# Kernel tuning notes

Hardware: AMD Instinct MI355X
Metric: run time of the kernel (lower is better)

Reference implementation:

```python
import jax, jax.numpy as jnp
import numpy as np


def _log_g(x):
    # log_g(x) = log(relu(x)+1) if x >= 0 else x
    return jnp.where(x >= 0, jnp.log1p(jnp.maximum(x, 0.0)), x)


def _min_gru(hg):
    # hg: [B, H, L] -> [B, H/2, L]
    h, gate = jnp.split(hg, 2, axis=1)
    log_coeffs = -jax.nn.softplus(gate)                    # log(1 - z)
    log_values = -jax.nn.softplus(-gate) + _log_g(h)       # log(z) + log g(h)
    a_star = jnp.cumsum(log_coeffs, axis=2)
    log_h0_plus_b_star = jax.lax.cumlogsumexp(log_values - a_star, axis=2)
    return jnp.exp(a_star + log_h0_plus_b_star)


def setup_inputs() -> dict:
    key = jax.random.key(0)
    B, H, L = 8, 512, 8192
    x = jax.random.normal(key, (B, H, L), dtype=jnp.float32)
    return {"x": x}


def reference(x) -> jnp.ndarray:
    # bidirectional minGRU: forward scan on first half of channels,
    # reversed scan on second half.
    fore, back = jnp.split(x, 2, axis=1)
    out_fore = _min_gru(fore)
    out_back = jnp.flip(_min_gru(jnp.flip(back, axis=2)), axis=2)
    return jnp.concatenate([out_fore, out_back], axis=1)  # [B, H/2, L]
```

## Files before the change

kernel.cpp:

```cpp
#include <hip/hip_runtime.h>
#include <math.h>


#define SEQ_L 8192
#define NTHREADS 256
#define PER_THREAD 8
#define TILE (NTHREADS * PER_THREAD)
#define NTILES (SEQ_L / TILE)

__global__ __launch_bounds__(NTHREADS) void mingru_scan_kernel(
    const float* __restrict__ x, float* __restrict__ out) {
    const int blk = blockIdx.x;
    const int dir = blk >> 10;
    const int s   = blk & 1023;
    const int b   = s >> 7;
    const int c   = s & 127;

    const int tid  = threadIdx.x;
    const int lane = tid & 63;
    const int wave = tid >> 6;

    const float* __restrict__ hrow = x + (size_t)((b * 512) + (dir * 256) + c) * SEQ_L;
    const float* __restrict__ grow = x + (size_t)((b * 512) + (dir * 256) + 128 + c) * SEQ_L;
    float* __restrict__ orow = out + (size_t)((b * 256) + (dir * 128) + c) * SEQ_L;

    __shared__ float sA[4];
    __shared__ float sB[4];

    float carry = 0.0f;

    for (int tile = 0; tile < NTILES; ++tile) {
        const int base = tile * TILE + tid * PER_THREAD;

        float hv[PER_THREAD], gv[PER_THREAD];
        if (dir == 0) {
            float4 h0 = *(const float4*)(hrow + base);
            float4 h1 = *(const float4*)(hrow + base + 4);
            float4 g0 = *(const float4*)(grow + base);
            float4 g1 = *(const float4*)(grow + base + 4);
            hv[0]=h0.x; hv[1]=h0.y; hv[2]=h0.z; hv[3]=h0.w;
            hv[4]=h1.x; hv[5]=h1.y; hv[6]=h1.z; hv[7]=h1.w;
            gv[0]=g0.x; gv[1]=g0.y; gv[2]=g0.z; gv[3]=g0.w;
            gv[4]=g1.x; gv[5]=g1.y; gv[6]=g1.z; gv[7]=g1.w;
        } else {
            const int p = SEQ_L - base - PER_THREAD;
            float4 h0 = *(const float4*)(hrow + p);
            float4 h1 = *(const float4*)(hrow + p + 4);
            float4 g0 = *(const float4*)(grow + p);
            float4 g1 = *(const float4*)(grow + p + 4);
            hv[0]=h1.w; hv[1]=h1.z; hv[2]=h1.y; hv[3]=h1.x;
            hv[4]=h0.w; hv[5]=h0.z; hv[6]=h0.y; hv[7]=h0.x;
            gv[0]=g1.w; gv[1]=g1.z; gv[2]=g1.y; gv[3]=g1.x;
            gv[4]=g0.w; gv[5]=g0.z; gv[6]=g0.y; gv[7]=g0.x;
        }

        float av[PER_THREAD], bv[PER_THREAD];
        float pa = 1.0f, pb = 0.0f;
#pragma unroll
        for (int j = 0; j < PER_THREAD; ++j) {
            const float gt = gv[j];
            const float e  = __expf(-fabsf(gt));
            const float r  = 1.0f / (1.0f + e);
            const float sn = e * r;
            const float sp = r;
            const float z  = (gt >= 0.0f) ? sp : sn;
            const float a  = (gt >= 0.0f) ? sn : sp;
            const float hh = hv[j];
            const float gf = (hh >= 0.0f) ? (hh + 1.0f) : __expf(hh);
            const float bb = z * gf;
            av[j] = a; bv[j] = bb;
            pb = a * pb + bb;
            pa = a * pa;
        }

#pragma unroll
        for (int d = 1; d < 64; d <<= 1) {
            const float oa = __shfl_up(pa, d);
            const float ob = __shfl_up(pb, d);
            if (lane >= d) {
                pb = pa * ob + pb;
                pa = pa * oa;
            }
        }

        if (lane == 63) { sA[wave] = pa; sB[wave] = pb; }
        __syncthreads();

        float st = carry;
        for (int w = 0; w < wave; ++w) st = sA[w] * st + sB[w];
        float ea = __shfl_up(pa, 1);
        float eb = __shfl_up(pb, 1);
        if (lane == 0) { ea = 1.0f; eb = 0.0f; }
        st = ea * st + eb;

        float ov[PER_THREAD];
        float H = st;
#pragma unroll
        for (int j = 0; j < PER_THREAD; ++j) {
            H = av[j] * H + bv[j];
            ov[j] = H;
        }

        if (dir == 0) {
            *(float4*)(orow + base)     = make_float4(ov[0], ov[1], ov[2], ov[3]);
            *(float4*)(orow + base + 4) = make_float4(ov[4], ov[5], ov[6], ov[7]);
        } else {
            const int p = SEQ_L - base - PER_THREAD;
            *(float4*)(orow + p)     = make_float4(ov[7], ov[6], ov[5], ov[4]);
            *(float4*)(orow + p + 4) = make_float4(ov[3], ov[2], ov[1], ov[0]);
        }

        float nc = carry;
#pragma unroll
        for (int w = 0; w < 4; ++w) nc = sA[w] * nc + sB[w];
        carry = nc;
        __syncthreads();
    }
}

extern "C" void kernel_launch(void* const* d_in, const int* in_sizes, int n_in,
                              void* d_out, int out_size, void* d_ws, size_t ws_size,
                              hipStream_t stream) {
    const float* x = (const float*)d_in[0];
    float* out = (float*)d_out;
    mingru_scan_kernel<<<2048, NTHREADS, 0, stream>>>(x, out);
}
```

Measured before the change: 228.5 us.

## Prefetch next tile, double-buffer wave totals, and apply carry with precomputed prefix products

Loads the next tile's h and gate values into registers before computing the current tile, so global memory latency overlaps with the scan math. The per-wave totals in shared memory are double-buffered, which removes the second barrier in each tile iteration. The final pass now uses the stored local prefix values plus carry times the prefix product, replacing a serial recurrence with independent FMAs. In exchange, register pressure rises from holding the prefetched float4s and the extra prefix arrays.

```diff
diff --git a/kernel.cpp b/kernel.cpp
--- a/kernel.cpp
+++ b/kernel.cpp
@@ -21,58 +21,69 @@
     const int wave = tid >> 6;
 
     const float* __restrict__ hrow = x + (size_t)((b * 512) + (dir * 256) + c) * SEQ_L;
-    const float* __restrict__ grow = x + (size_t)((b * 512) + (dir * 256) + 128 + c) * SEQ_L;
+    const float* __restrict__ grow = hrow + (size_t)128 * SEQ_L;
     float* __restrict__ orow = out + (size_t)((b * 256) + (dir * 128) + c) * SEQ_L;
 
-    __shared__ float sA[4];
-    __shared__ float sB[4];
+    __shared__ float sA[2][4];
+    __shared__ float sB[2][4];
 
     float carry = 0.0f;
 
-    for (int tile = 0; tile < NTILES; ++tile) {
-        const int base = tile * TILE + tid * PER_THREAD;
+    {
+    }
+    int base0 = tid * PER_THREAD;
+    int idx0  = dir ? (SEQ_L - base0 - PER_THREAD) : base0;
+    float4 nh0 = *(const float4*)(hrow + idx0);
+    float4 nh1 = *(const float4*)(hrow + idx0 + 4);
+    float4 ng0 = *(const float4*)(grow + idx0);
+    float4 ng1 = *(const float4*)(grow + idx0 + 4);
+
+#pragma unroll
+    for (int t = 0; t < NTILES; ++t) {
+        const float4 h0 = nh0, h1 = nh1, g0 = ng0, g1 = ng1;
+
+        if (t + 1 < NTILES) {
+            const int nb = (t + 1) * TILE + tid * PER_THREAD;
+            const int ni = dir ? (SEQ_L - nb - PER_THREAD) : nb;
+            nh0 = *(const float4*)(hrow + ni);
+            nh1 = *(const float4*)(hrow + ni + 4);
+            ng0 = *(const float4*)(grow + ni);
+            ng1 = *(const float4*)(grow + ni + 4);
+        }
 
         float hv[PER_THREAD], gv[PER_THREAD];
         if (dir == 0) {
-            float4 h0 = *(const float4*)(hrow + base);
-            float4 h1 = *(const float4*)(hrow + base + 4);
-            float4 g0 = *(const float4*)(grow + base);
-            float4 g1 = *(const float4*)(grow + base + 4);
             hv[0]=h0.x; hv[1]=h0.y; hv[2]=h0.z; hv[3]=h0.w;
             hv[4]=h1.x; hv[5]=h1.y; hv[6]=h1.z; hv[7]=h1.w;
             gv[0]=g0.x; gv[1]=g0.y; gv[2]=g0.z; gv[3]=g0.w;
             gv[4]=g1.x; gv[5]=g1.y; gv[6]=g1.z; gv[7]=g1.w;
         } else {
-            const int p = SEQ_L - base - PER_THREAD;
-            float4 h0 = *(const float4*)(hrow + p);
-            float4 h1 = *(const float4*)(hrow + p + 4);
-            float4 g0 = *(const float4*)(grow + p);
-            float4 g1 = *(const float4*)(grow + p + 4);
             hv[0]=h1.w; hv[1]=h1.z; hv[2]=h1.y; hv[3]=h1.x;
             hv[4]=h0.w; hv[5]=h0.z; hv[6]=h0.y; hv[7]=h0.x;
             gv[0]=g1.w; gv[1]=g1.z; gv[2]=g1.y; gv[3]=g1.x;
             gv[4]=g0.w; gv[5]=g0.z; gv[6]=g0.y; gv[7]=g0.x;
         }
 
-        float av[PER_THREAD], bv[PER_THREAD];
-        float pa = 1.0f, pb = 0.0f;
+        float pp[PER_THREAD], ov0[PER_THREAD];
+        float ca = 1.0f, cb = 0.0f;
 #pragma unroll
         for (int j = 0; j < PER_THREAD; ++j) {
             const float gt = gv[j];
             const float e  = __expf(-fabsf(gt));
             const float r  = 1.0f / (1.0f + e);
             const float sn = e * r;
-            const float sp = r;
-            const float z  = (gt >= 0.0f) ? sp : sn;
-            const float a  = (gt >= 0.0f) ? sn : sp;
+            const float z  = (gt >= 0.0f) ? r  : sn;
+            const float a  = (gt >= 0.0f) ? sn : r;
             const float hh = hv[j];
             const float gf = (hh >= 0.0f) ? (hh + 1.0f) : __expf(hh);
             const float bb = z * gf;
-            av[j] = a; bv[j] = bb;
-            pb = a * pb + bb;
-            pa = a * pa;
+            cb = a * cb + bb;
+            ca = a * ca;
+            ov0[j] = cb;
+            pp[j]  = ca;
         }
 
+        float pa = ca, pb = cb;
 #pragma unroll
         for (int d = 1; d < 64; d <<= 1) {
             const float oa = __shfl_up(pa, d);
@@ -83,24 +94,22 @@
             }
         }
 
-        if (lane == 63) { sA[wave] = pa; sB[wave] = pb; }
+        const int buf = t & 1;
+        if (lane == 63) { sA[buf][wave] = pa; sB[buf][wave] = pb; }
         __syncthreads();
 
         float st = carry;
-        for (int w = 0; w < wave; ++w) st = sA[w] * st + sB[w];
+        for (int w = 0; w < wave; ++w) st = sA[buf][w] * st + sB[buf][w];
         float ea = __shfl_up(pa, 1);
         float eb = __shfl_up(pb, 1);
         if (lane == 0) { ea = 1.0f; eb = 0.0f; }
         st = ea * st + eb;
 
         float ov[PER_THREAD];
-        float H = st;
 #pragma unroll
-        for (int j = 0; j < PER_THREAD; ++j) {
-            H = av[j] * H + bv[j];
-            ov[j] = H;
-        }
+        for (int j = 0; j < PER_THREAD; ++j) ov[j] = ov0[j] + st * pp[j];
 
+        const int base = t * TILE + tid * PER_THREAD;
         if (dir == 0) {
             *(float4*)(orow + base)     = make_float4(ov[0], ov[1], ov[2], ov[3]);
             *(float4*)(orow + base + 4) = make_float4(ov[4], ov[5], ov[6], ov[7]);
@@ -112,9 +121,8 @@
 
         float nc = carry;
 #pragma unroll
-        for (int w = 0; w < 4; ++w) nc = sA[w] * nc + sB[w];
+        for (int w = 0; w < 4; ++w) nc = sA[buf][w] * nc + sB[buf][w];
         carry = nc;
-        __syncthreads();
     }
 }
 
```

After: 209.6 us. 8.3% less time.
